# Kernel optimization log

Hardware: AMD Instinct MI355X
Metric: run time of the kernel (lower is better)

Reference implementation:

```python
import jax, jax.numpy as jnp
import numpy as np

B, C, Ci, N = 4, 512, 256, 4096
EPS = 1e-5

def _proj(x, W, b):
    # 1x1 Conv1d == per-node linear: x [B,C,N], W [O,C], b [O] -> [B,O,N]
    return jnp.einsum('oc,bcn->bon', W, x) + b[None, :, None]

def setup_inputs() -> dict:
    key = jax.random.key(0)
    ks = jax.random.split(key, 12)
    s_in = 1.0 / np.sqrt(C)
    s_ci = 1.0 / np.sqrt(Ci)
    return {
        'v':   jax.random.normal(ks[0], (B, C, N), jnp.float32),
        'Wg':  jax.random.normal(ks[1], (Ci, C), jnp.float32) * s_in,
        'bg':  jax.random.normal(ks[2], (Ci,), jnp.float32) * 0.01,
        'Wth': jax.random.normal(ks[3], (Ci, C), jnp.float32) * s_in,
        'bth': jax.random.normal(ks[4], (Ci,), jnp.float32) * 0.01,
        'Wph': jax.random.normal(ks[5], (Ci, C), jnp.float32) * s_in,
        'bph': jax.random.normal(ks[6], (Ci,), jnp.float32) * 0.01,
        'Ww':  jax.random.normal(ks[7], (C, Ci), jnp.float32) * s_ci,
        'bw':  jax.random.normal(ks[8], (C,), jnp.float32) * 0.01,
        'gamma': jax.random.uniform(ks[9], (C,), jnp.float32, 0.5, 1.5),
        'beta':  jax.random.normal(ks[10], (C,), jnp.float32) * 0.01,
    }

def reference(v, Wg, bg, Wth, bth, Wph, bph, Ww, bw, gamma, beta):
    # projections (1x1 convs)
    g_v = _proj(v, Wg, bg).transpose(0, 2, 1)      # [B,N,Ci]
    theta_v = _proj(v, Wth, bth).transpose(0, 2, 1)  # [B,N,Ci]
    phi_v = _proj(v, Wph, bph)                      # [B,Ci,N]
    # non-local affinity (no softmax), divided by N
    R = jnp.einsum('bnc,bcm->bnm', theta_v, phi_v) / N  # [B,N,N]
    y = jnp.einsum('bnm,bmc->bnc', R, g_v)              # [B,N,Ci]
    y = y.transpose(0, 2, 1)                            # [B,Ci,N]
    # W: 1x1 conv back to C, then BatchNorm1d (training-mode stats)
    Wy = _proj(y, Ww, bw)                               # [B,C,N]
    mean = jnp.mean(Wy, axis=(0, 2), keepdims=True)
    var = jnp.mean(jnp.square(Wy - mean), axis=(0, 2), keepdims=True)  # biased, as torch BN uses
    Wy_bn = (Wy - mean) * jax.lax.rsqrt(var + EPS)
    Wy_bn = Wy_bn * gamma[None, :, None] + beta[None, :, None]
    return Wy_bn + v
```

## Files before the change

### kernel.cpp

```cpp
#include <hip/hip_runtime.h>
#include <math.h>


#define B_  4
#define C_  512
#define CI_ 256
#define N_  4096

typedef __attribute__((ext_vector_type(8))) short bf16x8;
typedef __attribute__((ext_vector_type(4))) float f32x4;

#define G_OFF     0L
#define GH_OFF    1048576L
#define H_OFF     1572864L
#define P1_OFF    2621440L
#define SP_OFF    3145728L
#define P2_OFF    3407872L
#define MISC_OFF  3932160L
#define R_OFF     (MISC_OFF + 0)
#define BE_OFF    (MISC_OFF + 2048)
#define U1_OFF    (MISC_OFF + 4096)
#define U2_OFF    (MISC_OFF + 5120)
#define QF_OFF    (MISC_OFF + 6144)
#define MV_OFF    (MISC_OFF + 8192)
#define SC_OFF    (MISC_OFF + 10240)
#define SH_OFF    (MISC_OFF + 10752)
#define VH_OFF    3944448L
#define VL_OFF    8138752L
#define VTH_OFF   12333056L
#define WEH_OFF   16527360L
#define WEL_OFF   17051648L

__device__ __forceinline__ unsigned short f2bf(float f) {
    union { float f; unsigned int u; } a; a.f = f;
    unsigned int u = a.u;
    u += 0x7fffu + ((u >> 16) & 1u);
    return (unsigned short)(u >> 16);
}
__device__ __forceinline__ float bf2f(unsigned short s) {
    union { unsigned int u; float f; } a; a.u = ((unsigned int)s) << 16; return a.f;
}
__device__ __forceinline__ void gload_lds16(const char* g, char* l) {
    __builtin_amdgcn_global_load_lds(
        (const __attribute__((address_space(1))) unsigned int*)g,
        (__attribute__((address_space(3))) unsigned int*)l, 16, 0, 0);
}

__global__ __launch_bounds__(256) void cast_fused(
    const float* __restrict__ v, unsigned short* __restrict__ vh,
    unsigned short* __restrict__ vl, unsigned short* __restrict__ vth,
    float* __restrict__ r)
{
    __shared__ float tile[64][65];
    const int b = blockIdx.z;
    const int n0 = blockIdx.x * 64, c0 = blockIdx.y * 64;
    const int t = threadIdx.x, rq = t >> 4, cq = t & 15;
#pragma unroll
    for (int p = 0; p < 4; ++p) {
        int row = p * 16 + rq;
        long e = ((long)(b * C_ + c0 + row)) * N_ + n0 + cq * 4;
        float4 f = *(const float4*)&v[e];
        ushort4 h, l;
        h.x = f2bf(f.x); l.x = f2bf(f.x - bf2f(h.x));
        h.y = f2bf(f.y); l.y = f2bf(f.y - bf2f(h.y));
        h.z = f2bf(f.z); l.z = f2bf(f.z - bf2f(h.z));
        h.w = f2bf(f.w); l.w = f2bf(f.w - bf2f(h.w));
        *(ushort4*)&vh[e] = h;
        *(ushort4*)&vl[e] = l;
        tile[row][cq * 4 + 0] = f.x; tile[row][cq * 4 + 1] = f.y;
        tile[row][cq * 4 + 2] = f.z; tile[row][cq * 4 + 3] = f.w;
        float s = f.x + f.y + f.z + f.w;
        s += __shfl_xor(s, 1); s += __shfl_xor(s, 2);
        s += __shfl_xor(s, 4); s += __shfl_xor(s, 8);
        if (cq == 0) atomicAdd(&r[b * C_ + c0 + row], s);
    }
    __syncthreads();
#pragma unroll
    for (int p = 0; p < 4; ++p) {
        int nl = p * 16 + rq;
        float f0 = tile[cq * 4 + 0][nl], f1 = tile[cq * 4 + 1][nl];
        float f2 = tile[cq * 4 + 2][nl], f3 = tile[cq * 4 + 3][nl];
        ushort4 h;
        h.x = f2bf(f0); h.y = f2bf(f1); h.z = f2bf(f2); h.w = f2bf(f3);
        long e = ((long)(b * N_ + n0 + nl)) * C_ + c0 + cq * 4;
        *(ushort4*)&vth[e] = h;
    }
}

__global__ __launch_bounds__(256, 2) void gram_mfma(
    const unsigned short* __restrict__ vh, const unsigned short* __restrict__ vl,
    float* __restrict__ G)
{
    __shared__ char smem[49152];
    const int MT[10] = {0,1,1,2,2,2,3,3,3,3};
    const int NT[10] = {0,0,1,0,1,2,0,1,2,3};
    const int t = threadIdx.x, lane = t & 63, w = t >> 6;
    const int z = blockIdx.z, b = z >> 4, ch = z & 15;
    const long m0 = MT[blockIdx.x] * 128, n0 = NT[blockIdx.x] * 128;
    const long k0b = (long)ch * 512;
    const long stride = (long)N_ * 2;

    const char* vhm = (const char*)(vh + ((long)b * C_ + m0) * N_) + k0b;
    const char* vhn = (const char*)(vh + ((long)b * C_ + n0) * N_) + k0b;
    const char* vln = (const char*)(vl + ((long)b * C_ + n0) * N_) + k0b;
    char* AhL = smem; char* BhL = smem + 16384; char* BlL = smem + 32768;

    const char *g0, *g1; char *l0, *l1; int c0n;
    if (w == 0)      { g0 = vhm;                l0 = AhL;             c0n = 12; g1 = g0;  l1 = l0; }
    else if (w == 1) { g0 = vhm + 96 * stride;  l0 = AhL + 12 * 1024; c0n = 4;  g1 = vhn; l1 = BhL; }
    else if (w == 2) { g0 = vhn + 64 * stride;  l0 = BhL + 8 * 1024;  c0n = 8;  g1 = vln; l1 = BlL; }
    else             { g0 = vln + 32 * stride;  l0 = BlL + 4 * 1024;  c0n = 12; g1 = g0;  l1 = l0; }
    const long plane = (long)(lane >> 3) * stride + (((lane & 7) ^ (lane >> 3)) << 4);

    const int wr = w >> 1, wc = w & 1;
    const int l15 = lane & 15, hi4 = lane >> 4;
    const int swz = (l15 & 7) << 4;
    const int arow = (wr * 64 + l15) * 128;
    const int brow = (wc * 64 + l15) * 128;

    f32x4 acc[4][4];
#pragma unroll
    for (int mi = 0; mi < 4; ++mi)
#pragma unroll
        for (int nj = 0; nj < 4; ++nj) acc[mi][nj] = (f32x4){0.f, 0.f, 0.f, 0.f};

    for (int s = 0; s < 4; ++s) {
#pragma unroll
        for (int i = 0; i < 12; ++i) {
            const char* src; char* dst;
            if (i < c0n) { src = g0 + (long)i * 8 * stride;         dst = l0 + i * 1024; }
            else         { src = g1 + (long)(i - c0n) * 8 * stride; dst = l1 + (i - c0n) * 1024; }
            gload_lds16(src + plane + s * 128, dst);
        }
        __syncthreads();
#pragma unroll
        for (int kk = 0; kk < 2; ++kk) {
            const int off = (kk * 64 + hi4 * 16) ^ swz;
            bf16x8 ah[4], bh[4], bl[4];
#pragma unroll
            for (int mi = 0; mi < 4; ++mi)
                ah[mi] = *(const bf16x8*)(AhL + arow + mi * 2048 + off);
#pragma unroll
            for (int nj = 0; nj < 4; ++nj) {
                bh[nj] = *(const bf16x8*)(BhL + brow + nj * 2048 + off);
                bl[nj] = *(const bf16x8*)(BlL + brow + nj * 2048 + off);
            }
#pragma unroll
            for (int mi = 0; mi < 4; ++mi)
#pragma unroll
                for (int nj = 0; nj < 4; ++nj)
                    acc[mi][nj] = __builtin_amdgcn_mfma_f32_16x16x32_bf16(ah[mi], bh[nj], acc[mi][nj], 0, 0, 0);
#pragma unroll
            for (int mi = 0; mi < 4; ++mi)
#pragma unroll
                for (int nj = 0; nj < 4; ++nj)
                    acc[mi][nj] = __builtin_amdgcn_mfma_f32_16x16x32_bf16(ah[mi], bl[nj], acc[mi][nj], 0, 0, 0);
        }
        __syncthreads();
    }
#pragma unroll
    for (int mi = 0; mi < 4; ++mi)
#pragma unroll
        for (int nj = 0; nj < 4; ++nj)
#pragma unroll
            for (int rr = 0; rr < 4; ++rr) {
                long row = m0 + wr * 64 + mi * 16 + hi4 * 4 + rr;
                long col = n0 + wc * 64 + nj * 16 + l15;
                atomicAdd(&G[((long)b * C_ + row) * C_ + col], acc[mi][nj][rr]);
            }
}

__global__ __launch_bounds__(256) void mirror_g(float* __restrict__ G)
{
    const int J = blockIdx.x, I = blockIdx.y, b = blockIdx.z;
    if (I > J) return;
    __shared__ float tile[64][65];
    const int t = threadIdx.x, ty = t >> 4, tx = t & 15;
    float* Gb = G + (long)b * C_ * C_;
#pragma unroll
    for (int p = 0; p < 4; ++p) {
        int row = p * 16 + ty;
        *(float4*)&tile[row][tx * 4] =
            *(const float4*)&Gb[(long)(J * 64 + row) * C_ + I * 64 + tx * 4];
    }
    __syncthreads();
    if (I < J) {
#pragma unroll
        for (int p = 0; p < 4; ++p) {
            int row = p * 16 + ty;
            float4 o = make_float4(tile[tx * 4 + 0][row], tile[tx * 4 + 1][row],
                                   tile[tx * 4 + 2][row], tile[tx * 4 + 3][row]);
            *(float4*)&Gb[(long)(I * 64 + row) * C_ + J * 64 + tx * 4] = o;
        }
    } else {
#pragma unroll
        for (int p = 0; p < 4; ++p) {
            int row = p * 16 + ty;
            int i = I * 64 + row;
#pragma unroll
            for (int c = 0; c < 4; ++c) {
                int j = J * 64 + tx * 4 + c;
                if (i < j) Gb[(long)i * C_ + j] = tile[tx * 4 + c][row];
            }
        }
    }
}

__global__ __launch_bounds__(256) void g_cast(
    const float* __restrict__ G, unsigned short* __restrict__ Gh)
{
    long idx = (long)blockIdx.x * 256 + threadIdx.x;
    float4 f = ((const float4*)G)[idx];
    ushort4 h;
    h.x = f2bf(f.x); h.y = f2bf(f.y); h.z = f2bf(f.z); h.w = f2bf(f.w);
    ((ushort4*)Gh)[idx] = h;
}

__global__ __launch_bounds__(256, 2) void h_mfma(
    const unsigned short* __restrict__ weh, const unsigned short* __restrict__ wel,
    const unsigned short* __restrict__ Gh, float* __restrict__ H)
{
    __shared__ char smem[49152];
    const int t = threadIdx.x, lane = t & 63, w = t >> 6;
    const int b = blockIdx.z;
    const long m0 = blockIdx.y * 128, n0 = blockIdx.x * 128;
    const long S = (long)C_ * 2;

    const char* wehb = (const char*)(weh + ((long)b * C_ + m0) * C_);
    const char* welb = (const char*)(wel + ((long)b * C_ + m0) * C_);
    const char* ghb  = (const char*)(Gh  + ((long)b * C_ + n0) * C_);
    char* AhL = smem; char* AlL = smem + 16384; char* BhL = smem + 32768;

    const char *g0, *g1; char *l0, *l1; int c0n;
    if (w == 0)      { g0 = wehb;          l0 = AhL;             c0n = 12; g1 = g0;   l1 = l0; }
    else if (w == 1) { g0 = wehb + 96 * S; l0 = AhL + 12 * 1024; c0n = 4;  g1 = welb; l1 = AlL; }
    else if (w == 2) { g0 = welb + 64 * S; l0 = AlL + 8 * 1024;  c0n = 8;  g1 = ghb;  l1 = BhL; }
    else             { g0 = ghb + 32 * S;  l0 = BhL + 4 * 1024;  c0n = 12; g1 = g0;   l1 = l0; }
    const long plane = (long)(lane >> 3) * S + (((lane & 7) ^ (lane >> 3)) << 4);

    const int wr = w >> 1, wc = w & 1;
    const int l15 = lane & 15, hi4 = lane >> 4;
    const int swz = (l15 & 7) << 4;
    const int arow = (wr * 64 + l15) * 128;
    const int brow = (wc * 64 + l15) * 128;

    f32x4 acc[4][4];
#pragma unroll
    for (int mi = 0; mi < 4; ++mi)
#pragma unroll
        for (int nj = 0; nj < 4; ++nj) acc[mi][nj] = (f32x4){0.f, 0.f, 0.f, 0.f};

    for (int s = 0; s < 8; ++s) {
#pragma unroll
        for (int i = 0; i < 12; ++i) {
            const char* src; char* dst;
            if (i < c0n) { src = g0 + (long)i * 8 * S;         dst = l0 + i * 1024; }
            else         { src = g1 + (long)(i - c0n) * 8 * S; dst = l1 + (i - c0n) * 1024; }
            gload_lds16(src + plane + s * 128, dst);
        }
        __syncthreads();
#pragma unroll
        for (int kk = 0; kk < 2; ++kk) {
            const int off = (kk * 64 + hi4 * 16) ^ swz;
            bf16x8 ah[4], al[4], bh[4];
#pragma unroll
            for (int mi = 0; mi < 4; ++mi) {
                ah[mi] = *(const bf16x8*)(AhL + arow + mi * 2048 + off);
                al[mi] = *(const bf16x8*)(AlL + arow + mi * 2048 + off);
            }
#pragma unroll
            for (int nj = 0; nj < 4; ++nj)
                bh[nj] = *(const bf16x8*)(BhL + brow + nj * 2048 + off);
#pragma unroll
            for (int mi = 0; mi < 4; ++mi)
#pragma unroll
                for (int nj = 0; nj < 4; ++nj)
                    acc[mi][nj] = __builtin_amdgcn_mfma_f32_16x16x32_bf16(ah[mi], bh[nj], acc[mi][nj], 0, 0, 0);
#pragma unroll
            for (int mi = 0; mi < 4; ++mi)
#pragma unroll
                for (int nj = 0; nj < 4; ++nj)
                    acc[mi][nj] = __builtin_amdgcn_mfma_f32_16x16x32_bf16(al[mi], bh[nj], acc[mi][nj], 0, 0, 0);
        }
        __syncthreads();
    }
#pragma unroll
    for (int mi = 0; mi < 4; ++mi)
#pragma unroll
        for (int nj = 0; nj < 4; ++nj)
#pragma unroll
            for (int rr = 0; rr < 4; ++rr) {
                long row = m0 + wr * 64 + mi * 16 + hi4 * 4 + rr;
                long col = n0 + wc * 64 + nj * 16 + l15;
                H[((long)b * C_ + row) * C_ + col] = acc[mi][nj][rr];
            }
}

__global__ __launch_bounds__(256) void stats_k(
    const float* __restrict__ H, const unsigned short* __restrict__ weh,
    const unsigned short* __restrict__ wel, const float* __restrict__ r,
    float* __restrict__ QF, float* __restrict__ MV)
{
    const int bo = blockIdx.x;
    const int b = bo >> 9;
    const float* Hr = H + (long)bo * C_;
    const unsigned short* wh = weh + (long)bo * C_;
    const unsigned short* wl = wel + (long)bo * C_;
    const float* rb = r + b * C_;
    const int t = threadIdx.x;
    float qf = 0.f, mv = 0.f;
    for (int j = t; j < C_; j += 256) {
        float ws = bf2f(wh[j]) + bf2f(wl[j]);
        qf += Hr[j] * ws;
        mv += ws * rb[j];
    }
    qf += __shfl_xor(qf, 1);  mv += __shfl_xor(mv, 1);
    qf += __shfl_xor(qf, 2);  mv += __shfl_xor(mv, 2);
    qf += __shfl_xor(qf, 4);  mv += __shfl_xor(mv, 4);
    qf += __shfl_xor(qf, 8);  mv += __shfl_xor(mv, 8);
    qf += __shfl_xor(qf, 16); mv += __shfl_xor(mv, 16);
    qf += __shfl_xor(qf, 32); mv += __shfl_xor(mv, 32);
    __shared__ float sq[4], sm[4];
    if ((t & 63) == 0) { sq[t >> 6] = qf; sm[t >> 6] = mv; }
    __syncthreads();
    if (t == 0) {
        QF[bo] = sq[0] + sq[1] + sq[2] + sq[3];
        MV[bo] = sm[0] + sm[1] + sm[2] + sm[3];
    }
}

__global__ __launch_bounds__(512) void finalize_k(
    const float* __restrict__ QF, const float* __restrict__ MV,
    const float* __restrict__ be, const float* __restrict__ bw,
    const float* __restrict__ gamma, const float* __restrict__ beta,
    float* __restrict__ sc, float* __restrict__ sh)
{
    int o = threadIdx.x;
    float mean_acc = 0.f, ssq = 0.f;
    for (int b = 0; b < B_; ++b) {
        float bf = be[b * C_ + o] * (1.0f / (float)N_) + bw[o];
        float m = MV[b * C_ + o];
        float q = QF[b * C_ + o];
        mean_acc += m + (float)N_ * bf;
        ssq += q + 2.0f * bf * m + (float)N_ * bf * bf;
    }
    const float inv = 1.0f / ((float)B_ * (float)N_);
    float mean = mean_acc * inv;
    float var = ssq * inv - mean * mean;
    float s = gamma[o] * rsqrtf(var + 1e-5f);
    sc[o] = s;
    sh[o] = beta[o] - mean * s;
}

__global__ __launch_bounds__(256, 2) void wy_mfma(
    const unsigned short* __restrict__ weh, const unsigned short* __restrict__ wel,
    const unsigned short* __restrict__ vth,
    const float* __restrict__ be, const float* __restrict__ bw,
    const float* __restrict__ sc, const float* __restrict__ sh,
    const float* __restrict__ v, float* __restrict__ out)
{
    __shared__ char smem[49152];
    const int t = threadIdx.x, lane = t & 63, w = t >> 6;
    const int b = blockIdx.z;
    const long m0 = blockIdx.y * 128;
    const long n0 = blockIdx.x * 128;
    const long S = (long)C_ * 2;

    const char* wehb = (const char*)(weh + ((long)b * C_ + m0) * C_);
    const char* welb = (const char*)(wel + ((long)b * C_ + m0) * C_);
    const char* vhb  = (const char*)(vth + ((long)b * N_ + n0) * C_);
    char* AhL = smem; char* AlL = smem + 16384; char* BhL = smem + 32768;

    const char *g0, *g1; char *l0, *l1; int c0n;
    if (w == 0)      { g0 = wehb;          l0 = AhL;             c0n = 12; g1 = g0;   l1 = l0; }
    else if (w == 1) { g0 = wehb + 96 * S; l0 = AhL + 12 * 1024; c0n = 4;  g1 = welb; l1 = AlL; }
    else if (w == 2) { g0 = welb + 64 * S; l0 = AlL + 8 * 1024;  c0n = 8;  g1 = vhb;  l1 = BhL; }
    else             { g0 = vhb + 32 * S;  l0 = BhL + 4 * 1024;  c0n = 12; g1 = g0;   l1 = l0; }
    const long plane = (long)(lane >> 3) * S + (((lane & 7) ^ (lane >> 3)) << 4);

    const int wr = w >> 1, wc = w & 1;
    const int l15 = lane & 15, hi4 = lane >> 4;
    const int swz = (l15 & 7) << 4;
    const int arow = (wr * 64 + l15) * 128;
    const int brow = (wc * 64 + l15) * 128;

    f32x4 acc[4][4];
#pragma unroll
    for (int mi = 0; mi < 4; ++mi)
#pragma unroll
        for (int nj = 0; nj < 4; ++nj) acc[mi][nj] = (f32x4){0.f, 0.f, 0.f, 0.f};

    for (int s = 0; s < 8; ++s) {
#pragma unroll
        for (int i = 0; i < 12; ++i) {
            const char* src; char* dst;
            if (i < c0n) { src = g0 + (long)i * 8 * S;         dst = l0 + i * 1024; }
            else         { src = g1 + (long)(i - c0n) * 8 * S; dst = l1 + (i - c0n) * 1024; }
            gload_lds16(src + plane + s * 128, dst);
        }
        __syncthreads();
#pragma unroll
        for (int kk = 0; kk < 2; ++kk) {
            const int off = (kk * 64 + hi4 * 16) ^ swz;
            bf16x8 ah[4], al[4], bh[4];
#pragma unroll
            for (int mi = 0; mi < 4; ++mi) {
                ah[mi] = *(const bf16x8*)(AhL + arow + mi * 2048 + off);
                al[mi] = *(const bf16x8*)(AlL + arow + mi * 2048 + off);
            }
#pragma unroll
            for (int nj = 0; nj < 4; ++nj)
                bh[nj] = *(const bf16x8*)(BhL + brow + nj * 2048 + off);
#pragma unroll
            for (int mi = 0; mi < 4; ++mi)
#pragma unroll
                for (int nj = 0; nj < 4; ++nj)
                    acc[mi][nj] = __builtin_amdgcn_mfma_f32_16x16x32_bf16(ah[mi], bh[nj], acc[mi][nj], 0, 0, 0);
#pragma unroll
            for (int mi = 0; mi < 4; ++mi)
#pragma unroll
                for (int nj = 0; nj < 4; ++nj)
                    acc[mi][nj] = __builtin_amdgcn_mfma_f32_16x16x32_bf16(al[mi], bh[nj], acc[mi][nj], 0, 0, 0);
        }
        __syncthreads();
    }

#pragma unroll
    for (int mi = 0; mi < 4; ++mi) {
#pragma unroll
        for (int rr = 0; rr < 4; ++rr) {
            long o = m0 + wr * 64 + mi * 16 + hi4 * 4 + rr;
            float bf = be[b * C_ + o] * (1.0f / (float)N_) + bw[o];
            float s_c = sc[o], s_h = sh[o];
#pragma unroll
            for (int nj = 0; nj < 4; ++nj) {
                long n = n0 + wc * 64 + nj * 16 + l15;
                long e = ((long)b * C_ + o) * N_ + n;
                float val = acc[mi][nj][rr] + bf;
                out[e] = val * s_c + s_h + v[e];
            }
        }
    }
}

__global__ __launch_bounds__(256) void gemm_nn(
    const float* __restrict__ A, long sA, int lda,
    const float* __restrict__ Bm, long sB, int ldb,
    float* __restrict__ Cm, long sC, int ldc,
    int K, float scale, int mode,
    const float* __restrict__ bth, float* __restrict__ be,
    unsigned short* __restrict__ weh, unsigned short* __restrict__ wel)
{
    int b = blockIdx.z;
    const float* Ab = A + (long)b * sA;
    const float* Bb = Bm + (long)b * sB;
    int i0 = blockIdx.y * 64, j0 = blockIdx.x * 64;

    __shared__ __align__(16) float As[16][64];
    __shared__ __align__(16) float Bs[16][64];

    int t = threadIdx.x, tx = t & 15, ty = t >> 4;
    int am = t >> 2, akq = (t & 3) << 2;
    int bk = t >> 4, bn4 = (t & 15) << 2;

    float acc[4][4];
#pragma unroll
    for (int r = 0; r < 4; ++r)
#pragma unroll
        for (int c = 0; c < 4; ++c) acc[r][c] = 0.f;

    for (int k0 = 0; k0 < K; k0 += 16) {
        float4 va = *(const float4*)&Ab[(long)(i0 + am) * lda + k0 + akq];
        As[akq + 0][am] = va.x; As[akq + 1][am] = va.y;
        As[akq + 2][am] = va.z; As[akq + 3][am] = va.w;
        *(float4*)&Bs[bk][bn4] = *(const float4*)&Bb[(long)(k0 + bk) * ldb + j0 + bn4];
        __syncthreads();
#pragma unroll
        for (int k = 0; k < 16; ++k) {
            float4 a4 = *(float4*)&As[k][ty * 4];
            float4 b4 = *(float4*)&Bs[k][tx * 4];
            float a[4]  = {a4.x, a4.y, a4.z, a4.w};
            float bb[4] = {b4.x, b4.y, b4.z, b4.w};
#pragma unroll
            for (int r = 0; r < 4; ++r)
#pragma unroll
                for (int c = 0; c < 4; ++c)
                    acc[r][c] += a[r] * bb[c];
        }
        __syncthreads();
    }

    if (mode == 2) {
#pragma unroll
        for (int r = 0; r < 4; ++r) {
            int o = i0 + ty * 4 + r, p = j0 + tx * 4;
            ushort4 h, l;
            float f0 = acc[r][0] * scale, f1 = acc[r][1] * scale;
            float f2 = acc[r][2] * scale, f3 = acc[r][3] * scale;
            h.x = f2bf(f0); l.x = f2bf(f0 - bf2f(h.x));
            h.y = f2bf(f1); l.y = f2bf(f1 - bf2f(h.y));
            h.z = f2bf(f2); l.z = f2bf(f2 - bf2f(h.z));
            h.w = f2bf(f3); l.w = f2bf(f3 - bf2f(h.w));
            long e = (((long)b * C_ + o) * C_ + p) >> 2;
            ((ushort4*)weh)[e] = h;
            ((ushort4*)wel)[e] = l;
        }
        return;
    }
    float* Cb = Cm + (long)b * sC;
#pragma unroll
    for (int r = 0; r < 4; ++r) {
        float4 o0 = make_float4(acc[r][0] * scale, acc[r][1] * scale,
                                acc[r][2] * scale, acc[r][3] * scale);
        *(float4*)&Cb[(long)(i0 + ty * 4 + r) * ldc + j0 + tx * 4] = o0;
    }
    if (mode == 1) {
#pragma unroll
        for (int r = 0; r < 4; ++r) {
            float pr = acc[r][0] * bth[j0 + tx * 4 + 0]
                     + acc[r][1] * bth[j0 + tx * 4 + 1]
                     + acc[r][2] * bth[j0 + tx * 4 + 2]
                     + acc[r][3] * bth[j0 + tx * 4 + 3];
            pr += __shfl_xor(pr, 1); pr += __shfl_xor(pr, 2);
            pr += __shfl_xor(pr, 4); pr += __shfl_xor(pr, 8);
            if (tx == 0) atomicAdd(&be[b * C_ + i0 + ty * 4 + r], pr);
        }
    }
}

__global__ __launch_bounds__(256) void gemm_nt_sp(
    const float* __restrict__ P1, const float* __restrict__ Wph,
    float* __restrict__ SP, const float* __restrict__ u1,
    const float* __restrict__ u2, const float* __restrict__ bg,
    const float* __restrict__ bph)
{
    int b = blockIdx.z;
    const float* Ab = P1 + (long)b * (CI_ * C_);
    int i0 = blockIdx.y * 64, j0 = blockIdx.x * 64;

    __shared__ __align__(16) float As[16][64];
    __shared__ __align__(16) float Bs[16][64];

    int t = threadIdx.x, tx = t & 15, ty = t >> 4;
    int lr = t >> 2, lk = (t & 3) << 2;

    float acc[4][4];
#pragma unroll
    for (int r = 0; r < 4; ++r)
#pragma unroll
        for (int c = 0; c < 4; ++c) acc[r][c] = 0.f;

    for (int kt = 0; kt < C_; kt += 16) {
        float4 va = *(const float4*)&Ab[(long)(i0 + lr) * C_ + kt + lk];
        float4 vb = *(const float4*)&Wph[(long)(j0 + lr) * C_ + kt + lk];
        As[lk + 0][lr] = va.x; As[lk + 1][lr] = va.y; As[lk + 2][lr] = va.z; As[lk + 3][lr] = va.w;
        Bs[lk + 0][lr] = vb.x; Bs[lk + 1][lr] = vb.y; Bs[lk + 2][lr] = vb.z; Bs[lk + 3][lr] = vb.w;
        __syncthreads();
#pragma unroll
        for (int k = 0; k < 16; ++k) {
            float4 a4 = *(float4*)&As[k][ty * 4];
            float4 b4 = *(float4*)&Bs[k][tx * 4];
            float a[4]  = {a4.x, a4.y, a4.z, a4.w};
            float bb[4] = {b4.x, b4.y, b4.z, b4.w};
#pragma unroll
            for (int r = 0; r < 4; ++r)
#pragma unroll
                for (int c = 0; c < 4; ++c)
                    acc[r][c] += a[r] * bb[c];
        }
        __syncthreads();
    }
    float* Cb = SP + (long)b * (CI_ * CI_);
#pragma unroll
    for (int r = 0; r < 4; ++r) {
        int cr = i0 + ty * 4 + r;
        float u1v = u1[b * CI_ + cr], bgv = bg[cr];
        float4 o0;
        float* po = (float*)&o0;
#pragma unroll
        for (int c = 0; c < 4; ++c) {
            int ic = j0 + tx * 4 + c;
            po[c] = acc[r][c] + u1v * bph[ic] + bgv * (u2[b * CI_ + ic] + (float)N_ * bph[ic]);
        }
        *(float4*)&Cb[(long)cr * CI_ + j0 + tx * 4] = o0;
    }
}

__global__ __launch_bounds__(256) void rank1_prep(
    const float* __restrict__ Wg, const float* __restrict__ Wph,
    const float* __restrict__ r, float* __restrict__ u1, float* __restrict__ u2)
{
    int blk = blockIdx.x;
    int b = blk >> 2, q = blk & 3;
    int t = threadIdx.x;
    int c = q * 64 + (t >> 2);
    int kq = t & 3;
    const float* rb = r + b * C_;
    float s1 = 0.f, s2 = 0.f;
    for (int k = kq * 128; k < kq * 128 + 128; k += 4) {
        float4 wg = *(const float4*)&Wg[(long)c * C_ + k];
        float4 wp = *(const float4*)&Wph[(long)c * C_ + k];
        float4 rv = *(const float4*)&rb[k];
        s1 += wg.x * rv.x + wg.y * rv.y + wg.z * rv.z + wg.w * rv.w;
        s2 += wp.x * rv.x + wp.y * rv.y + wp.z * rv.z + wp.w * rv.w;
    }
    s1 += __shfl_xor(s1, 1); s2 += __shfl_xor(s2, 1);
    s1 += __shfl_xor(s1, 2); s2 += __shfl_xor(s2, 2);
    if (kq == 0) {
        u1[b * CI_ + c] = s1;
        u2[b * CI_ + c] = s2;
    }
}

extern "C" void kernel_launch(void* const* d_in, const int* in_sizes, int n_in,
                              void* d_out, int out_size, void* d_ws, size_t ws_size,
                              hipStream_t stream)
{
    const float* v     = (const float*)d_in[0];
    const float* Wg    = (const float*)d_in[1];
    const float* bg    = (const float*)d_in[2];
    const float* Wth   = (const float*)d_in[3];
    const float* bth   = (const float*)d_in[4];
    const float* Wph   = (const float*)d_in[5];
    const float* bph   = (const float*)d_in[6];
    const float* Ww    = (const float*)d_in[7];
    const float* bw    = (const float*)d_in[8];
    const float* gamma = (const float*)d_in[9];
    const float* beta  = (const float*)d_in[10];
    float* out = (float*)d_out;
    float* ws  = (float*)d_ws;

    float* G    = ws + G_OFF;
    float* H    = ws + H_OFF;
    float* P1   = ws + P1_OFF;
    float* SP   = ws + SP_OFF;
    float* P2   = ws + P2_OFF;
    float* r    = ws + R_OFF;
    float* be   = ws + BE_OFF;
    float* u1   = ws + U1_OFF;
    float* u2   = ws + U2_OFF;
    float* QF   = ws + QF_OFF;
    float* MV   = ws + MV_OFF;
    float* sc   = ws + SC_OFF;
    float* sh   = ws + SH_OFF;
    unsigned short* Gh  = (unsigned short*)(ws + GH_OFF);
    unsigned short* vh  = (unsigned short*)(ws + VH_OFF);
    unsigned short* vl  = (unsigned short*)(ws + VL_OFF);
    unsigned short* vth = (unsigned short*)(ws + VTH_OFF);
    unsigned short* weh = (unsigned short*)(ws + WEH_OFF);
    unsigned short* wel = (unsigned short*)(ws + WEL_OFF);

    hipMemsetAsync(G, 0, 1048576 * sizeof(float), stream);
    hipMemsetAsync(r, 0, 4096 * sizeof(float), stream);

    cast_fused<<<dim3(64, 8, 4), 256, 0, stream>>>(v, vh, vl, vth, r);

    gram_mfma<<<dim3(10, 1, 64), 256, 0, stream>>>(vh, vl, G);
    mirror_g<<<dim3(8, 8, 4), 256, 0, stream>>>(G);

    rank1_prep<<<16, 256, 0, stream>>>(Wg, Wph, r, u1, u2);

    gemm_nn<<<dim3(8, 4, 4), 256, 0, stream>>>(
        Wg, 0, C_, G, (long)C_ * C_, C_, P1, (long)CI_ * C_, C_,
        C_, 1.0f, 0, nullptr, nullptr, nullptr, nullptr);

    gemm_nt_sp<<<dim3(4, 4, 4), 256, 0, stream>>>(P1, Wph, SP, u1, u2, bg, bph);

    gemm_nn<<<dim3(4, 8, 4), 256, 0, stream>>>(
        Ww, 0, CI_, SP, (long)CI_ * CI_, CI_, P2, (long)C_ * CI_, CI_,
        CI_, 1.0f, 1, bth, be, nullptr, nullptr);

    gemm_nn<<<dim3(8, 8, 4), 256, 0, stream>>>(
        P2, (long)C_ * CI_, CI_, Wth, 0, C_, nullptr, 0, 0,
        CI_, 1.0f / (float)N_, 2, nullptr, nullptr, weh, wel);

    g_cast<<<1024, 256, 0, stream>>>(G, Gh);
    h_mfma<<<dim3(4, 4, 4), 256, 0, stream>>>(weh, wel, Gh, H);
    stats_k<<<2048, 256, 0, stream>>>(H, weh, wel, r, QF, MV);
    finalize_k<<<1, 512, 0, stream>>>(QF, MV, be, bw, gamma, beta, sc, sh);

    wy_mfma<<<dim3(32, 4, 4), 256, 0, stream>>>(weh, wel, vth, be, bw, sc, sh, v, out);
}
```

Baseline: 309.8 us.

## Replace atomic Gram accumulation with split-K partials and fused reduce-mirror-cast

The Gram kernel now uses 8 K-chunks of 1024 instead of 16 chunks of 512. Each block writes its 128x128 partial tile to a workspace buffer instead of doing float atomicAdds into G. A new reduce_mirror kernel sums the 8 partials, writes both G and its bf16 copy Gh, and mirrors the upper triangle into the lower. This removes the G memset, the mirror kernel, the cast kernel and the atomic traffic. It costs about 5 MB of partial writes and reads, and the transposed stores in the reduce kernel are uncoalesced.

```diff
diff --git a/kernel.cpp b/kernel.cpp
--- a/kernel.cpp
+++ b/kernel.cpp
@@ -30,6 +30,7 @@
 #define VTH_OFF   12333056L
 #define WEH_OFF   16527360L
 #define WEL_OFF   17051648L
+#define GP_OFF    17575936L
 
 __device__ __forceinline__ unsigned short f2bf(float f) {
     union { float f; unsigned int u; } a; a.f = f;
@@ -89,15 +90,15 @@
 
 __global__ __launch_bounds__(256, 2) void gram_mfma(
     const unsigned short* __restrict__ vh, const unsigned short* __restrict__ vl,
-    float* __restrict__ G)
+    float* __restrict__ Gp)
 {
     __shared__ char smem[49152];
     const int MT[10] = {0,1,1,2,2,2,3,3,3,3};
     const int NT[10] = {0,0,1,0,1,2,0,1,2,3};
     const int t = threadIdx.x, lane = t & 63, w = t >> 6;
-    const int z = blockIdx.z, b = z >> 4, ch = z & 15;
+    const int z = blockIdx.z, b = z >> 3, ch = z & 7;
     const long m0 = MT[blockIdx.x] * 128, n0 = NT[blockIdx.x] * 128;
-    const long k0b = (long)ch * 512;
+    const long k0b = (long)ch * 1024;
     const long stride = (long)N_ * 2;
 
     const char* vhm = (const char*)(vh + ((long)b * C_ + m0) * N_) + k0b;
@@ -124,7 +125,7 @@
 #pragma unroll
         for (int nj = 0; nj < 4; ++nj) acc[mi][nj] = (f32x4){0.f, 0.f, 0.f, 0.f};
 
-    for (int s = 0; s < 4; ++s) {
+    for (int s = 0; s < 8; ++s) {
 #pragma unroll
         for (int i = 0; i < 12; ++i) {
             const char* src; char* dst;
@@ -158,62 +159,69 @@
         }
         __syncthreads();
     }
+    float* gp = Gp + (((long)b * 10 + blockIdx.x) * 8 + ch) * 16384;
 #pragma unroll
     for (int mi = 0; mi < 4; ++mi)
 #pragma unroll
         for (int nj = 0; nj < 4; ++nj)
 #pragma unroll
             for (int rr = 0; rr < 4; ++rr) {
-                long row = m0 + wr * 64 + mi * 16 + hi4 * 4 + rr;
-                long col = n0 + wc * 64 + nj * 16 + l15;
-                atomicAdd(&G[((long)b * C_ + row) * C_ + col], acc[mi][nj][rr]);
-            }
-}
-
-__global__ __launch_bounds__(256) void mirror_g(float* __restrict__ G)
-{
-    const int J = blockIdx.x, I = blockIdx.y, b = blockIdx.z;
-    if (I > J) return;
-    __shared__ float tile[64][65];
-    const int t = threadIdx.x, ty = t >> 4, tx = t & 15;
+                int row = wr * 64 + mi * 16 + hi4 * 4 + rr;
+                int col = wc * 64 + nj * 16 + l15;
+                gp[row * 128 + col] = acc[mi][nj][rr];
+            }
+}
+
+__global__ __launch_bounds__(256) void reduce_mirror(
+    const float* __restrict__ Gp, float* __restrict__ G,
+    unsigned short* __restrict__ Gh)
+{
+    const int MT[10] = {0,1,1,2,2,2,3,3,3,3};
+    const int NT[10] = {0,0,1,0,1,2,0,1,2,3};
+    const int strip = blockIdx.x, x = blockIdx.y, b = blockIdx.z;
+    const int I = MT[x], J = NT[x];
+    const float* base = Gp + ((long)(b * 10 + x) * 8) * 16384;
     float* Gb = G + (long)b * C_ * C_;
-#pragma unroll
-    for (int p = 0; p < 4; ++p) {
-        int row = p * 16 + ty;
-        *(float4*)&tile[row][tx * 4] =
-            *(const float4*)&Gb[(long)(J * 64 + row) * C_ + I * 64 + tx * 4];
-    }
-    __syncthreads();
-    if (I < J) {
-#pragma unroll
-        for (int p = 0; p < 4; ++p) {
-            int row = p * 16 + ty;
-            float4 o = make_float4(tile[tx * 4 + 0][row], tile[tx * 4 + 1][row],
-                                   tile[tx * 4 + 2][row], tile[tx * 4 + 3][row]);
-            *(float4*)&Gb[(long)(I * 64 + row) * C_ + J * 64 + tx * 4] = o;
-        }
-    } else {
-#pragma unroll
-        for (int p = 0; p < 4; ++p) {
-            int row = p * 16 + ty;
-            int i = I * 64 + row;
-#pragma unroll
-            for (int c = 0; c < 4; ++c) {
-                int j = J * 64 + tx * 4 + c;
-                if (i < j) Gb[(long)i * C_ + j] = tile[tx * 4 + c][row];
-            }
-        }
-    }
-}
-
-__global__ __launch_bounds__(256) void g_cast(
-    const float* __restrict__ G, unsigned short* __restrict__ Gh)
-{
-    long idx = (long)blockIdx.x * 256 + threadIdx.x;
-    float4 f = ((const float4*)G)[idx];
-    ushort4 h;
-    h.x = f2bf(f.x); h.y = f2bf(f.y); h.z = f2bf(f.z); h.w = f2bf(f.w);
-    ((ushort4*)Gh)[idx] = h;
+    unsigned short* Ghb = Gh + (long)b * C_ * C_;
+    const int t = threadIdx.x;
+    const int c = strip * 32 + (t & 7) * 4;
+    const int r0 = t >> 3;
+#pragma unroll
+    for (int rp = 0; rp < 4; ++rp) {
+        int row = rp * 32 + r0;
+        float4 s = make_float4(0.f, 0.f, 0.f, 0.f);
+#pragma unroll
+        for (int ch = 0; ch < 8; ++ch) {
+            float4 p = *(const float4*)&base[ch * 16384 + row * 128 + c];
+            s.x += p.x; s.y += p.y; s.z += p.z; s.w += p.w;
+        }
+        long rg = I * 128 + row, cg = J * 128 + c;
+        ushort4 h;
+        h.x = f2bf(s.x); h.y = f2bf(s.y); h.z = f2bf(s.z); h.w = f2bf(s.w);
+        if (I != J) {
+            *(float4*)&Gb[rg * C_ + cg]   = s;
+            *(ushort4*)&Ghb[rg * C_ + cg] = h;
+            const float sv[4] = {s.x, s.y, s.z, s.w};
+            const unsigned short hv[4] = {h.x, h.y, h.z, h.w};
+#pragma unroll
+            for (int j = 0; j < 4; ++j) {
+                Gb[(cg + j) * C_ + rg]  = sv[j];
+                Ghb[(cg + j) * C_ + rg] = hv[j];
+            }
+        } else {
+            const float sv[4] = {s.x, s.y, s.z, s.w};
+            const unsigned short hv[4] = {h.x, h.y, h.z, h.w};
+#pragma unroll
+            for (int j = 0; j < 4; ++j) {
+                if (c + j <= row) {
+                    Gb[rg * C_ + cg + j]    = sv[j];
+                    Ghb[rg * C_ + cg + j]   = hv[j];
+                    Gb[(cg + j) * C_ + rg]  = sv[j];
+                    Ghb[(cg + j) * C_ + rg] = hv[j];
+                }
+            }
+        }
+    }
 }
 
 __global__ __launch_bounds__(256, 2) void h_mfma(
@@ -643,6 +651,7 @@
     float* MV   = ws + MV_OFF;
     float* sc   = ws + SC_OFF;
     float* sh   = ws + SH_OFF;
+    float* Gp   = ws + GP_OFF;
     unsigned short* Gh  = (unsigned short*)(ws + GH_OFF);
     unsigned short* vh  = (unsigned short*)(ws + VH_OFF);
     unsigned short* vl  = (unsigned short*)(ws + VL_OFF);
@@ -650,13 +659,12 @@
     unsigned short* weh = (unsigned short*)(ws + WEH_OFF);
     unsigned short* wel = (unsigned short*)(ws + WEL_OFF);
 
-    hipMemsetAsync(G, 0, 1048576 * sizeof(float), stream);
     hipMemsetAsync(r, 0, 4096 * sizeof(float), stream);
 
     cast_fused<<<dim3(64, 8, 4), 256, 0, stream>>>(v, vh, vl, vth, r);
 
-    gram_mfma<<<dim3(10, 1, 64), 256, 0, stream>>>(vh, vl, G);
-    mirror_g<<<dim3(8, 8, 4), 256, 0, stream>>>(G);
+    gram_mfma<<<dim3(10, 1, 32), 256, 0, stream>>>(vh, vl, Gp);
+    reduce_mirror<<<dim3(4, 10, 4), 256, 0, stream>>>(Gp, G, Gh);
 
     rank1_prep<<<16, 256, 0, stream>>>(Wg, Wph, r, u1, u2);
 
@@ -674,7 +682,6 @@
         P2, (long)C_ * CI_, CI_, Wth, 0, C_, nullptr, 0, 0,
         CI_, 1.0f / (float)N_, 2, nullptr, nullptr, weh, wel);
 
-    g_cast<<<1024, 256, 0, stream>>>(G, Gh);
     h_mfma<<<dim3(4, 4, 4), 256, 0, stream>>>(weh, wel, Gh, H);
     stats_k<<<2048, 256, 0, stream>>>(H, weh, wel, r, QF, MV);
     finalize_k<<<1, 512, 0, stream>>>(QF, MV, be, bw, gamma, beta, sc, sh);
```

New measurement: 288.3 us. 7.0% less time.
